# Performance work log

Hardware: AMD Instinct MI355X
Metric: run time of the kernel (lower is better)

Reference implementation:

```python
import jax, jax.numpy as jnp
import numpy as np

N = 4096
D = 256
THRESH = 0.04  # default threshold arg of MultiLayerGCN.forward


def setup_inputs() -> dict:
    key = jax.random.key(0)
    ks = jax.random.split(key, 6)
    A = jax.random.normal(ks[0], (N, N), dtype=jnp.float32)
    features = jax.random.normal(ks[1], (N, D), dtype=jnp.float32)
    s = 0.02
    W1 = jax.random.normal(ks[2], (D, D), dtype=jnp.float32) * s
    b1 = jax.random.normal(ks[3], (D,), dtype=jnp.float32) * s
    W2 = jax.random.normal(ks[4], (D, D), dtype=jnp.float32) * s
    b2 = jax.random.normal(ks[5], (D,), dtype=jnp.float32) * s
    return {"A": A, "features": features, "W1": W1, "b1": b1, "W2": W2, "b2": b2}


def _graph_conv(C, out_isqrt, in_isqrt, h, W, b):
    # DGL GraphConv, norm='both': scale src by out_deg^-1/2, aggregate over
    # edges u->v (rst[v] = sum_u C[u,v] * h[u]), scale dst by in_deg^-1/2.
    h = (h * out_isqrt[:, None]) @ W            # [N, out]
    agg = jnp.einsum('uv,ud->vd', C, h)          # C^T @ h, honoring edge direction
    return agg * in_isqrt[:, None] + b


def reference(A, features, W1, b1, W2, b2):
    dt = features.dtype
    mask = (A >= THRESH).astype(dt)
    # add_edges(nodes, nodes) adds self loops on top of surviving diagonal -> counts
    C = mask + jnp.eye(A.shape[0], dtype=dt)
    out_deg = jnp.maximum(C.sum(axis=1), 1.0)    # clamp(min=1) as in DGL
    in_deg = jnp.maximum(C.sum(axis=0), 1.0)
    out_isqrt = jax.lax.rsqrt(out_deg)
    in_isqrt = jax.lax.rsqrt(in_deg)
    h1 = jax.nn.relu(_graph_conv(C, out_isqrt, in_isqrt, features, W1, b1))
    h2 = jax.nn.relu(_graph_conv(C, out_isqrt, in_isqrt, h1, W2, b2))
    return (h1, h2)
```

## Files before the change

### kernel.cpp

```cpp
#include <hip/hip_runtime.h>
#include <stdint.h>

#define NN 4096
#define DD 256
#define TH 0.04f

typedef __attribute__((ext_vector_type(4))) float f32x4;
typedef __attribute__((ext_vector_type(16))) float f32x16;
typedef __attribute__((ext_vector_type(8))) short s16x8;
typedef unsigned short us;

__device__ __forceinline__ us f2bf(float f) {
  union { float f; uint32_t u; } x; x.f = f;
  uint32_t u = x.u;
  return (us)((u + 0x7FFFu + ((u >> 16) & 1u)) >> 16);
}
__device__ __forceinline__ float bf2f(us h) {
  union { uint32_t u; float f; } x; x.u = ((uint32_t)h) << 16;
  return x.f;
}

__device__ __forceinline__ void hw_block(const float* __restrict__ H,
                                         const float* __restrict__ W,
                                         int u0,
                                         us* __restrict__ hWb,
                                         us* __restrict__ hWbP,
                                         char* smem) {
  us (*hs)[264] = reinterpret_cast<us(*)[264]>(smem);
  us (*wt)[34]  = reinterpret_cast<us(*)[34]>(smem + 16 * 264 * 2);
  us (*lt)[260] = reinterpret_cast<us(*)[260]>(smem + 16 * 264 * 2 + 256 * 34 * 2);
  const int t = threadIdx.x;
#pragma unroll
  for (int rep = 0; rep < 4; ++rep) {
    const int flat = rep * 256 + t;
    const int row = flat >> 6, c4 = (flat & 63) * 4;
    f32x4 v = *reinterpret_cast<const f32x4*>(H + (size_t)(u0 + row) * DD + c4);
    uint2 pw;
    pw.x = (uint32_t)f2bf(v[0]) | ((uint32_t)f2bf(v[1]) << 16);
    pw.y = (uint32_t)f2bf(v[2]) | ((uint32_t)f2bf(v[3]) << 16);
    *reinterpret_cast<uint2*>(&hs[row][c4]) = pw;
  }
  const int lane = t & 63, w = t >> 6, l15 = lane & 15, l4 = lane >> 4;
  const f32x4 z = {0.f, 0.f, 0.f, 0.f};
  f32x4 acc[4];
#pragma unroll
  for (int jn = 0; jn < 4; ++jn) acc[jn] = z;
#pragma unroll 1
  for (int ks = 0; ks < 8; ++ks) {
    __syncthreads();
#pragma unroll
    for (int rr = 0; rr < 8; ++rr) {
      const int flat = rr * 256 + t;
      const int k = flat >> 6, d0 = (flat & 63) * 4;
      f32x4 wv = *reinterpret_cast<const f32x4*>(W + (size_t)(ks * 32 + k) * DD + d0);
      wt[d0 + 0][k] = f2bf(wv[0]);
      wt[d0 + 1][k] = f2bf(wv[1]);
      wt[d0 + 2][k] = f2bf(wv[2]);
      wt[d0 + 3][k] = f2bf(wv[3]);
    }
    __syncthreads();
    s16x8 af = *reinterpret_cast<const s16x8*>(&hs[l15][ks * 32 + l4 * 8]);
#pragma unroll
    for (int jn = 0; jn < 4; ++jn) {
      const int dt = w * 4 + jn;
      s16x8 bf = *reinterpret_cast<const s16x8*>(&wt[dt * 16 + l15][l4 * 8]);
      acc[jn] = __builtin_amdgcn_mfma_f32_16x16x32_bf16(af, bf, acc[jn], 0, 0, 0);
    }
  }
#pragma unroll
  for (int jn = 0; jn < 4; ++jn) {
    const int d = w * 64 + jn * 16 + l15;
#pragma unroll
    for (int r = 0; r < 4; ++r) {
      const int ul = l4 * 4 + r;
      us hv = f2bf(acc[jn][r]);
      hWb[(size_t)(u0 + ul) * DD + d] = hv;
      lt[ul][d] = hv;
    }
  }
  __syncthreads();
  const int sg = u0 >> 4;
#pragma unroll
  for (int cc = 0; cc < 2; ++cc) {
    const int c = t * 2 + cc;
    const int dt = c >> 6, lc = c & 63;
    const int ub = (lc >> 5) * 8;
    const int d = dt * 32 + (lc & 31);
    uint4 val;
    val.x = (uint32_t)lt[ub + 0][d] | ((uint32_t)lt[ub + 1][d] << 16);
    val.y = (uint32_t)lt[ub + 2][d] | ((uint32_t)lt[ub + 3][d] << 16);
    val.z = (uint32_t)lt[ub + 4][d] | ((uint32_t)lt[ub + 5][d] << 16);
    val.w = (uint32_t)lt[ub + 6][d] | ((uint32_t)lt[ub + 7][d] << 16);
    *reinterpret_cast<uint4*>(hWbP + ((size_t)dt * 256 + sg) * 512 + lc * 8) = val;
  }
}

__global__ __launch_bounds__(256) void k_scanhw1(const float* __restrict__ A,
                                                 const float* __restrict__ feat,
                                                 const float* __restrict__ W1,
                                                 us* __restrict__ bitsT,
                                                 unsigned char* __restrict__ colpart,
                                                 float* __restrict__ oif,
                                                 us* __restrict__ oib,
                                                 us* __restrict__ hWb,
                                                 us* __restrict__ hWbP) {
  __shared__ __align__(16) char smem[34176];
  if (blockIdx.x >= 512) {
    hw_block(feat, W1, (blockIdx.x - 512) * 16, hWb, hWbP, smem);
    return;
  }
  us* lds16 = reinterpret_cast<us*>(smem);
  const int t = threadIdx.x, b = blockIdx.x;
  const int u0 = b * 8;
  uint32_t cs[16];
#pragma unroll
  for (int k = 0; k < 16; ++k) cs[k] = 0;
#pragma unroll
  for (int rb = 0; rb < 2; ++rb) {
    f32x4 a[4][4];
#pragma unroll
    for (int r = 0; r < 4; ++r) {
      const f32x4* p = reinterpret_cast<const f32x4*>(A + (size_t)(u0 + rb * 4 + r) * NN + t * 16);
#pragma unroll
      for (int c = 0; c < 4; ++c) a[r][c] = p[c];
    }
#pragma unroll
    for (int r = 0; r < 4; ++r) {
      uint32_t m = 0;
#pragma unroll
      for (int c = 0; c < 4; ++c)
#pragma unroll
        for (int j = 0; j < 4; ++j) m |= (a[r][c][j] >= TH ? 1u : 0u) << (c * 4 + j);
      lds16[t * 8 + rb * 4 + r] = (us)m;
#pragma unroll
      for (int k = 0; k < 16; ++k) cs[k] += (m >> k) & 1u;
    }
  }
  uint4 pk;
  pk.x = cs[0]  | (cs[1]  << 8) | (cs[2]  << 16) | (cs[3]  << 24);
  pk.y = cs[4]  | (cs[5]  << 8) | (cs[6]  << 16) | (cs[7]  << 24);
  pk.z = cs[8]  | (cs[9]  << 8) | (cs[10] << 16) | (cs[11] << 24);
  pk.w = cs[12] | (cs[13] << 8) | (cs[14] << 16) | (cs[15] << 24);
  *reinterpret_cast<uint4*>(colpart + (size_t)b * 4096 + t * 16) = pk;
  __syncthreads();
  uint4 wv4 = *reinterpret_cast<const uint4*>(&lds16[t * 8]);
  *reinterpret_cast<uint4*>(bitsT + (size_t)t * 4096 + u0) = wv4;
  if (t < 64) {
    const int r = t >> 3, part = t & 7;
    uint32_t s = 0;
#pragma unroll
    for (int wv = part * 32; wv < part * 32 + 32; ++wv)
      s += (uint32_t)__popc((uint32_t)lds16[wv * 8 + r]);
    s += __shfl_down(s, 4, 8);
    s += __shfl_down(s, 2, 8);
    s += __shfl_down(s, 1, 8);
    if (part == 0) {
      float val = rsqrtf((float)(s + 1u));
      oif[u0 + r] = val;
      oib[u0 + r] = f2bf(val);
    }
  }
}

__global__ __launch_bounds__(256) void k_hw(const float* __restrict__ H,
                                            const float* __restrict__ W,
                                            us* __restrict__ hWb,
                                            us* __restrict__ hWbP) {
  __shared__ __align__(16) char smem[34176];
  hw_block(H, W, blockIdx.x * 16, hWb, hWbP, smem);
}

__global__ __launch_bounds__(512, 2) void k_spmm(const us* __restrict__ bitsT,
                                                 const us* __restrict__ hWbP,
                                                 const us* __restrict__ hWb,
                                                 const float* __restrict__ oif,
                                                 const us* __restrict__ oib,
                                                 const unsigned char* __restrict__ colpart,
                                                 float* __restrict__ ii_g,
                                                 const float* __restrict__ bias,
                                                 float* __restrict__ dst,
                                                 int doii) {
  __shared__ float lds[4 * 64 * 68];
  __shared__ float ii_s[64];
  const int t = threadIdx.x, bb = blockIdx.x;
  const int lane = t & 63, w = t >> 6;
  const int kc = w >> 1, dn = w & 1;
  const int xcd = bb & 7, jj = bb >> 3;
  const int vt = xcd * 8 + (jj >> 2), dq = jj & 3;
  const int V0 = vt * 64, D0 = dq * 64;

  if (doii) {
    uint32_t* sc = reinterpret_cast<uint32_t*>(lds);
    const int v4 = t & 15, c = t >> 4;
    uint32_t s0 = 0, s1 = 0;
#pragma unroll 4
    for (int r = 0; r < 16; ++r) {
      uint32_t x = *reinterpret_cast<const uint32_t*>(colpart + (size_t)(c * 16 + r) * 4096 + V0 + v4 * 4);
      s0 += x & 0x00FF00FFu;
      s1 += (x >> 8) & 0x00FF00FFu;
    }
    sc[(c * 16 + v4) * 2] = s0;
    sc[(c * 16 + v4) * 2 + 1] = s1;
    __syncthreads();
    if (t < 64) {
      const int v4b = t >> 2, sub = t & 3;
      const int reg = sub & 1, hi = sub >> 1;
      uint32_t s = 0;
#pragma unroll
      for (int cc = 0; cc < 32; ++cc)
        s += (sc[(cc * 16 + v4b) * 2 + reg] >> (hi * 16)) & 0xFFFFu;
      float val = rsqrtf((float)(s + 1u));
      ii_s[t] = val;
      ii_g[V0 + t] = val;
    }
    __syncthreads();
  } else {
    if (t < 64) ii_s[t] = ii_g[V0 + t];
    __syncthreads();
  }

  const int l31 = lane & 31, l5 = lane >> 5;
  const uint32_t sh = lane & 15;
  const int wsel = (lane >> 4) & 1;
  const us* A0 = bitsT + (size_t)(vt * 4 + wsel) * 4096 + kc * 1024 + l5 * 8;
  const us* A1 = bitsT + (size_t)(vt * 4 + 2 + wsel) * 4096 + kc * 1024 + l5 * 8;
  const us* Ob = oib + kc * 1024 + l5 * 8;
  const int dt = dq * 2 + dn;
  const us* Bp = hWbP + ((size_t)dt * 256 + kc * 64) * 512 + lane * 8;

  f32x16 acc0, acc1;
#pragma unroll
  for (int q = 0; q < 16; ++q) { acc0[q] = 0.f; acc1[q] = 0.f; }

  uint4 h0a = *reinterpret_cast<const uint4*>(A0);
  uint4 h1a = *reinterpret_cast<const uint4*>(A1);
  s16x8 oa = *reinterpret_cast<const s16x8*>(Ob);
  s16x8 pa = *reinterpret_cast<const s16x8*>(Bp);
  uint4 h0b = *reinterpret_cast<const uint4*>(A0 + 16);
  uint4 h1b = *reinterpret_cast<const uint4*>(A1 + 16);
  s16x8 ob = *reinterpret_cast<const s16x8*>(Ob + 16);
  s16x8 pb = *reinterpret_cast<const s16x8*>(Bp + 512);

#define XPAND(AF, H, O)                                                        \
  {                                                                            \
    const uint32_t* ou = reinterpret_cast<const uint32_t*>(&(O));              \
    uint32_t m_;                                                               \
    m_ = (((H).x >> sh) & 0x10001u) * 0xFFFFu; AF.u[0] = ou[0] & m_;           \
    m_ = (((H).y >> sh) & 0x10001u) * 0xFFFFu; AF.u[1] = ou[1] & m_;           \
    m_ = (((H).z >> sh) & 0x10001u) * 0xFFFFu; AF.u[2] = ou[2] & m_;           \
    m_ = (((H).w >> sh) & 0x10001u) * 0xFFFFu; AF.u[3] = ou[3] & m_;           \
  }

#pragma unroll 1
  for (int it = 0; it < 32; ++it) {
    {
      union { s16x8 v; uint32_t u[4]; } af0, af1;
      XPAND(af0, h0a, oa);
      XPAND(af1, h1a, oa);
      acc0 = __builtin_amdgcn_mfma_f32_32x32x16_bf16(af0.v, pa, acc0, 0, 0, 0);
      acc1 = __builtin_amdgcn_mfma_f32_32x32x16_bf16(af1.v, pa, acc1, 0, 0, 0);
      const int sA = (it * 2 + 2) & 63;
      h0a = *reinterpret_cast<const uint4*>(A0 + sA * 16);
      h1a = *reinterpret_cast<const uint4*>(A1 + sA * 16);
      oa = *reinterpret_cast<const s16x8*>(Ob + sA * 16);
      pa = *reinterpret_cast<const s16x8*>(Bp + (size_t)sA * 512);
    }
    {
      union { s16x8 v; uint32_t u[4]; } af0, af1;
      XPAND(af0, h0b, ob);
      XPAND(af1, h1b, ob);
      acc0 = __builtin_amdgcn_mfma_f32_32x32x16_bf16(af0.v, pb, acc0, 0, 0, 0);
      acc1 = __builtin_amdgcn_mfma_f32_32x32x16_bf16(af1.v, pb, acc1, 0, 0, 0);
      const int sB = (it * 2 + 3) & 63;
      h0b = *reinterpret_cast<const uint4*>(A0 + sB * 16);
      h1b = *reinterpret_cast<const uint4*>(A1 + sB * 16);
      ob = *reinterpret_cast<const s16x8*>(Ob + sB * 16);
      pb = *reinterpret_cast<const s16x8*>(Bp + (size_t)sB * 512);
    }
  }
#undef XPAND

  float* buf = lds + (size_t)kc * (64 * 68);
#pragma unroll
  for (int reg = 0; reg < 16; ++reg) {
    const int row = (reg & 3) + 8 * (reg >> 2) + 4 * l5;
    buf[row * 68 + dn * 32 + l31] = acc0[reg];
    buf[(32 + row) * 68 + dn * 32 + l31] = acc1[reg];
  }
  __syncthreads();

  const int vloc = t >> 3, d8 = (t & 7) * 8;
  const int v = V0 + vloc;
  const float* base = lds + vloc * 68 + d8;
  f32x4 s0v = *reinterpret_cast<const f32x4*>(base);
  f32x4 s1v = *reinterpret_cast<const f32x4*>(base + 4);
#pragma unroll
  for (int q = 1; q < 4; ++q) {
    s0v += *reinterpret_cast<const f32x4*>(base + q * (64 * 68));
    s1v += *reinterpret_cast<const f32x4*>(base + q * (64 * 68) + 4);
  }
  union { s16x8 v; us u[8]; } self;
  self.v = *reinterpret_cast<const s16x8*>(hWb + (size_t)v * DD + D0 + d8);
  const float iv = ii_s[vloc];
  const float ov = oif[v];
  const f32x4 bi0 = *reinterpret_cast<const f32x4*>(bias + D0 + d8);
  const f32x4 bi1 = *reinterpret_cast<const f32x4*>(bias + D0 + d8 + 4);
  f32x4 o0, o1;
#pragma unroll
  for (int e = 0; e < 4; ++e) {
    o0[e] = fmaxf((s0v[e] + ov * bf2f(self.u[e])) * iv + bi0[e], 0.f);
    o1[e] = fmaxf((s1v[e] + ov * bf2f(self.u[e + 4])) * iv + bi1[e], 0.f);
  }
  f32x4* po = reinterpret_cast<f32x4*>(dst + (size_t)v * DD + D0 + d8);
  po[0] = o0; po[1] = o1;
}

extern "C" void kernel_launch(void* const* d_in, const int* in_sizes, int n_in,
                              void* d_out, int out_size, void* d_ws, size_t ws_size,
                              hipStream_t stream) {
  const float* A    = (const float*)d_in[0];
  const float* feat = (const float*)d_in[1];
  const float* W1   = (const float*)d_in[2];
  const float* b1   = (const float*)d_in[3];
  const float* W2   = (const float*)d_in[4];
  const float* b2   = (const float*)d_in[5];
  float* out = (float*)d_out;
  char* ws = (char*)d_ws;

  us*            bitsT   = (us*)ws;
  unsigned char* colpart = (unsigned char*)(ws + (2u << 20));
  us*            hWbP    = (us*)(ws + (4u << 20));
  us*            hWb     = (us*)(ws + (6u << 20));
  float*         oif     = (float*)(ws + (8u << 20));
  us*            oib     = (us*)(ws + (8u << 20) + (16u << 10));
  float*         ii_g    = (float*)(ws + (8u << 20) + (24u << 10));

  k_scanhw1<<<768, 256, 0, stream>>>(A, feat, W1, bitsT, colpart, oif, oib, hWb, hWbP);
  k_spmm<<<256, 512, 0, stream>>>(bitsT, hWbP, hWb, oif, oib, colpart, ii_g, b1, out, 1);
  k_hw<<<256, 256, 0, stream>>>(out, W2, hWb, hWbP);
  k_spmm<<<256, 512, 0, stream>>>(bitsT, hWbP, hWb, oif, oib, colpart, ii_g, b2,
                                  out + (size_t)NN * DD, 0);
}
```

Before: 86.33 us.

## Pre-pack W2 into MFMA fragments and share A-fragment across two D tiles in SpMM

The first kernel now also converts W2 to bf16 in MFMA B-fragment order, and the layer-2 h·W kernel reads these fragments straight from global memory instead of staging and transposing W through LDS. The SpMM kernel is re-tiled so each wave builds one expanded adjacency fragment and reuses it for two D sub-tiles. This halves the bit-expansion ALU work and uses a 4-deep prefetch ring. The trade-off is more registers for the deeper prefetch and more global B-fragment loads per wave.

```diff
diff --git a/kernel.cpp b/kernel.cpp
--- a/kernel.cpp
+++ b/kernel.cpp
@@ -20,12 +20,12 @@
   return x.f;
 }
 
-__device__ __forceinline__ void hw_block(const float* __restrict__ H,
-                                         const float* __restrict__ W,
-                                         int u0,
-                                         us* __restrict__ hWb,
-                                         us* __restrict__ hWbP,
-                                         char* smem) {
+__device__ __forceinline__ void hw_selfstage(const float* __restrict__ H,
+                                             const float* __restrict__ W,
+                                             int u0,
+                                             us* __restrict__ hWb,
+                                             us* __restrict__ hWbP,
+                                             char* smem) {
   us (*hs)[264] = reinterpret_cast<us(*)[264]>(smem);
   us (*wt)[34]  = reinterpret_cast<us(*)[34]>(smem + 16 * 264 * 2);
   us (*lt)[260] = reinterpret_cast<us(*)[260]>(smem + 16 * 264 * 2 + 256 * 34 * 2);
@@ -98,15 +98,17 @@
 __global__ __launch_bounds__(256) void k_scanhw1(const float* __restrict__ A,
                                                  const float* __restrict__ feat,
                                                  const float* __restrict__ W1,
+                                                 const float* __restrict__ W2,
                                                  us* __restrict__ bitsT,
                                                  unsigned char* __restrict__ colpart,
                                                  float* __restrict__ oif,
                                                  us* __restrict__ oib,
                                                  us* __restrict__ hWb,
-                                                 us* __restrict__ hWbP) {
+                                                 us* __restrict__ hWbP,
+                                                 us* __restrict__ W2TbP) {
   __shared__ __align__(16) char smem[34176];
   if (blockIdx.x >= 512) {
-    hw_block(feat, W1, (blockIdx.x - 512) * 16, hWb, hWbP, smem);
+    hw_selfstage(feat, W1, (blockIdx.x - 512) * 16, hWb, hWbP, smem);
     return;
   }
   us* lds16 = reinterpret_cast<us*>(smem);
@@ -160,14 +162,81 @@
       oib[u0 + r] = f2bf(val);
     }
   }
-}
-
-__global__ __launch_bounds__(256) void k_hw(const float* __restrict__ H,
-                                            const float* __restrict__ W,
-                                            us* __restrict__ hWb,
-                                            us* __restrict__ hWbP) {
-  __shared__ __align__(16) char smem[34176];
-  hw_block(H, W, blockIdx.x * 16, hWb, hWbP, smem);
+  if (b < 16) {
+    const int base = b * 4096 + t * 16;
+#pragma unroll
+    for (int e = 0; e < 16; ++e) {
+      const int idx = base + e;
+      const int frag = idx >> 9, pos = idx & 511;
+      const int lc = pos >> 3, j = pos & 7;
+      const int dt = frag >> 3, ks = frag & 7;
+      const int k = ks * 32 + (lc >> 4) * 8 + j;
+      const int d = dt * 16 + (lc & 15);
+      W2TbP[idx] = f2bf(W2[k * 256 + d]);
+    }
+  }
+}
+
+__global__ __launch_bounds__(256) void k_hw2(const float* __restrict__ H,
+                                             const us* __restrict__ WP,
+                                             us* __restrict__ hWb,
+                                             us* __restrict__ hWbP) {
+  __shared__ us hs[16][264];
+  __shared__ us lt[16][260];
+  const int t = threadIdx.x;
+  const int u0 = blockIdx.x * 16;
+#pragma unroll
+  for (int rep = 0; rep < 4; ++rep) {
+    const int flat = rep * 256 + t;
+    const int row = flat >> 6, c4 = (flat & 63) * 4;
+    f32x4 v = *reinterpret_cast<const f32x4*>(H + (size_t)(u0 + row) * DD + c4);
+    uint2 pw;
+    pw.x = (uint32_t)f2bf(v[0]) | ((uint32_t)f2bf(v[1]) << 16);
+    pw.y = (uint32_t)f2bf(v[2]) | ((uint32_t)f2bf(v[3]) << 16);
+    *reinterpret_cast<uint2*>(&hs[row][c4]) = pw;
+  }
+  __syncthreads();
+  const int lane = t & 63, w = t >> 6, l15 = lane & 15, l4 = lane >> 4;
+  const f32x4 z = {0.f, 0.f, 0.f, 0.f};
+  f32x4 acc[4];
+#pragma unroll
+  for (int jn = 0; jn < 4; ++jn) acc[jn] = z;
+#pragma unroll
+  for (int ks = 0; ks < 8; ++ks) {
+    s16x8 af = *reinterpret_cast<const s16x8*>(&hs[l15][ks * 32 + l4 * 8]);
+#pragma unroll
+    for (int jn = 0; jn < 4; ++jn) {
+      const int dt = w * 4 + jn;
+      s16x8 bf = *reinterpret_cast<const s16x8*>(WP + ((size_t)dt * 8 + ks) * 512 + lane * 8);
+      acc[jn] = __builtin_amdgcn_mfma_f32_16x16x32_bf16(af, bf, acc[jn], 0, 0, 0);
+    }
+  }
+#pragma unroll
+  for (int jn = 0; jn < 4; ++jn) {
+    const int d = w * 64 + jn * 16 + l15;
+#pragma unroll
+    for (int r = 0; r < 4; ++r) {
+      const int ul = l4 * 4 + r;
+      us hv = f2bf(acc[jn][r]);
+      hWb[(size_t)(u0 + ul) * DD + d] = hv;
+      lt[ul][d] = hv;
+    }
+  }
+  __syncthreads();
+  const int sg = u0 >> 4;
+#pragma unroll
+  for (int cc = 0; cc < 2; ++cc) {
+    const int c = t * 2 + cc;
+    const int dt = c >> 6, lc = c & 63;
+    const int ub = (lc >> 5) * 8;
+    const int d = dt * 32 + (lc & 31);
+    uint4 val;
+    val.x = (uint32_t)lt[ub + 0][d] | ((uint32_t)lt[ub + 1][d] << 16);
+    val.y = (uint32_t)lt[ub + 2][d] | ((uint32_t)lt[ub + 3][d] << 16);
+    val.z = (uint32_t)lt[ub + 4][d] | ((uint32_t)lt[ub + 5][d] << 16);
+    val.w = (uint32_t)lt[ub + 6][d] | ((uint32_t)lt[ub + 7][d] << 16);
+    *reinterpret_cast<uint4*>(hWbP + ((size_t)dt * 256 + sg) * 512 + lc * 8) = val;
+  }
 }
 
 __global__ __launch_bounds__(512, 2) void k_spmm(const us* __restrict__ bitsT,
@@ -184,7 +253,7 @@
   __shared__ float ii_s[64];
   const int t = threadIdx.x, bb = blockIdx.x;
   const int lane = t & 63, w = t >> 6;
-  const int kc = w >> 1, dn = w & 1;
+  const int mi = w & 1, kc = w >> 1;
   const int xcd = bb & 7, jj = bb >> 3;
   const int vt = xcd * 8 + (jj >> 2), dq = jj & 3;
   const int V0 = vt * 64, D0 = dq * 64;
@@ -221,71 +290,52 @@
 
   const int l31 = lane & 31, l5 = lane >> 5;
   const uint32_t sh = lane & 15;
-  const int wsel = (lane >> 4) & 1;
-  const us* A0 = bitsT + (size_t)(vt * 4 + wsel) * 4096 + kc * 1024 + l5 * 8;
-  const us* A1 = bitsT + (size_t)(vt * 4 + 2 + wsel) * 4096 + kc * 1024 + l5 * 8;
+  const int wvl = vt * 4 + mi * 2 + ((lane >> 4) & 1);
+  const us* Ab = bitsT + (size_t)wvl * 4096 + kc * 1024 + l5 * 8;
   const us* Ob = oib + kc * 1024 + l5 * 8;
-  const int dt = dq * 2 + dn;
-  const us* Bp = hWbP + ((size_t)dt * 256 + kc * 64) * 512 + lane * 8;
+  const us* Bp0 = hWbP + ((size_t)(dq * 2 + 0) * 256 + kc * 64) * 512 + lane * 8;
+  const us* Bp1 = hWbP + ((size_t)(dq * 2 + 1) * 256 + kc * 64) * 512 + lane * 8;
 
   f32x16 acc0, acc1;
 #pragma unroll
   for (int q = 0; q < 16; ++q) { acc0[q] = 0.f; acc1[q] = 0.f; }
 
-  uint4 h0a = *reinterpret_cast<const uint4*>(A0);
-  uint4 h1a = *reinterpret_cast<const uint4*>(A1);
-  s16x8 oa = *reinterpret_cast<const s16x8*>(Ob);
-  s16x8 pa = *reinterpret_cast<const s16x8*>(Bp);
-  uint4 h0b = *reinterpret_cast<const uint4*>(A0 + 16);
-  uint4 h1b = *reinterpret_cast<const uint4*>(A1 + 16);
-  s16x8 ob = *reinterpret_cast<const s16x8*>(Ob + 16);
-  s16x8 pb = *reinterpret_cast<const s16x8*>(Bp + 512);
-
-#define XPAND(AF, H, O)                                                        \
-  {                                                                            \
-    const uint32_t* ou = reinterpret_cast<const uint32_t*>(&(O));              \
-    uint32_t m_;                                                               \
-    m_ = (((H).x >> sh) & 0x10001u) * 0xFFFFu; AF.u[0] = ou[0] & m_;           \
-    m_ = (((H).y >> sh) & 0x10001u) * 0xFFFFu; AF.u[1] = ou[1] & m_;           \
-    m_ = (((H).z >> sh) & 0x10001u) * 0xFFFFu; AF.u[2] = ou[2] & m_;           \
-    m_ = (((H).w >> sh) & 0x10001u) * 0xFFFFu; AF.u[3] = ou[3] & m_;           \
+  uint4 h[4]; s16x8 o[4], p0[4], p1[4];
+#pragma unroll
+  for (int sl = 0; sl < 4; ++sl) {
+    h[sl]  = *reinterpret_cast<const uint4*>(Ab + sl * 16);
+    o[sl]  = *reinterpret_cast<const s16x8*>(Ob + sl * 16);
+    p0[sl] = *reinterpret_cast<const s16x8*>(Bp0 + (size_t)sl * 512);
+    p1[sl] = *reinterpret_cast<const s16x8*>(Bp1 + (size_t)sl * 512);
   }
 
 #pragma unroll 1
-  for (int it = 0; it < 32; ++it) {
-    {
-      union { s16x8 v; uint32_t u[4]; } af0, af1;
-      XPAND(af0, h0a, oa);
-      XPAND(af1, h1a, oa);
-      acc0 = __builtin_amdgcn_mfma_f32_32x32x16_bf16(af0.v, pa, acc0, 0, 0, 0);
-      acc1 = __builtin_amdgcn_mfma_f32_32x32x16_bf16(af1.v, pa, acc1, 0, 0, 0);
-      const int sA = (it * 2 + 2) & 63;
-      h0a = *reinterpret_cast<const uint4*>(A0 + sA * 16);
-      h1a = *reinterpret_cast<const uint4*>(A1 + sA * 16);
-      oa = *reinterpret_cast<const s16x8*>(Ob + sA * 16);
-      pa = *reinterpret_cast<const s16x8*>(Bp + (size_t)sA * 512);
-    }
-    {
-      union { s16x8 v; uint32_t u[4]; } af0, af1;
-      XPAND(af0, h0b, ob);
-      XPAND(af1, h1b, ob);
-      acc0 = __builtin_amdgcn_mfma_f32_32x32x16_bf16(af0.v, pb, acc0, 0, 0, 0);
-      acc1 = __builtin_amdgcn_mfma_f32_32x32x16_bf16(af1.v, pb, acc1, 0, 0, 0);
-      const int sB = (it * 2 + 3) & 63;
-      h0b = *reinterpret_cast<const uint4*>(A0 + sB * 16);
-      h1b = *reinterpret_cast<const uint4*>(A1 + sB * 16);
-      ob = *reinterpret_cast<const s16x8*>(Ob + sB * 16);
-      pb = *reinterpret_cast<const s16x8*>(Bp + (size_t)sB * 512);
-    }
-  }
-#undef XPAND
+  for (int it = 0; it < 16; ++it) {
+#pragma unroll
+    for (int sl = 0; sl < 4; ++sl) {
+      union { s16x8 v; uint32_t u[4]; } af;
+      const uint32_t* ou = reinterpret_cast<const uint32_t*>(&o[sl]);
+      uint32_t m;
+      m = ((h[sl].x >> sh) & 0x10001u) * 0xFFFFu; af.u[0] = ou[0] & m;
+      m = ((h[sl].y >> sh) & 0x10001u) * 0xFFFFu; af.u[1] = ou[1] & m;
+      m = ((h[sl].z >> sh) & 0x10001u) * 0xFFFFu; af.u[2] = ou[2] & m;
+      m = ((h[sl].w >> sh) & 0x10001u) * 0xFFFFu; af.u[3] = ou[3] & m;
+      acc0 = __builtin_amdgcn_mfma_f32_32x32x16_bf16(af.v, p0[sl], acc0, 0, 0, 0);
+      acc1 = __builtin_amdgcn_mfma_f32_32x32x16_bf16(af.v, p1[sl], acc1, 0, 0, 0);
+      const int ns = (it * 4 + sl + 4) & 63;
+      h[sl]  = *reinterpret_cast<const uint4*>(Ab + ns * 16);
+      o[sl]  = *reinterpret_cast<const s16x8*>(Ob + ns * 16);
+      p0[sl] = *reinterpret_cast<const s16x8*>(Bp0 + (size_t)ns * 512);
+      p1[sl] = *reinterpret_cast<const s16x8*>(Bp1 + (size_t)ns * 512);
+    }
+  }
 
   float* buf = lds + (size_t)kc * (64 * 68);
 #pragma unroll
   for (int reg = 0; reg < 16; ++reg) {
     const int row = (reg & 3) + 8 * (reg >> 2) + 4 * l5;
-    buf[row * 68 + dn * 32 + l31] = acc0[reg];
-    buf[(32 + row) * 68 + dn * 32 + l31] = acc1[reg];
+    buf[(mi * 32 + row) * 68 + l31] = acc0[reg];
+    buf[(mi * 32 + row) * 68 + 32 + l31] = acc1[reg];
   }
   __syncthreads();
 
@@ -331,13 +381,15 @@
   unsigned char* colpart = (unsigned char*)(ws + (2u << 20));
   us*            hWbP    = (us*)(ws + (4u << 20));
   us*            hWb     = (us*)(ws + (6u << 20));
-  float*         oif     = (float*)(ws + (8u << 20));
-  us*            oib     = (us*)(ws + (8u << 20) + (16u << 10));
-  float*         ii_g    = (float*)(ws + (8u << 20) + (24u << 10));
-
-  k_scanhw1<<<768, 256, 0, stream>>>(A, feat, W1, bitsT, colpart, oif, oib, hWb, hWbP);
+  us*            W2TbP   = (us*)(ws + (8u << 20));
+  float*         oif     = (float*)(ws + (8u << 20) + (1u << 17));
+  us*            oib     = (us*)(ws + (8u << 20) + (1u << 17) + (16u << 10));
+  float*         ii_g    = (float*)(ws + (8u << 20) + (1u << 17) + (24u << 10));
+
+  k_scanhw1<<<768, 256, 0, stream>>>(A, feat, W1, W2, bitsT, colpart, oif, oib,
+                                     hWb, hWbP, W2TbP);
   k_spmm<<<256, 512, 0, stream>>>(bitsT, hWbP, hWb, oif, oib, colpart, ii_g, b1, out, 1);
-  k_hw<<<256, 256, 0, stream>>>(out, W2, hWb, hWbP);
+  k_hw2<<<256, 256, 0, stream>>>(out, W2TbP, hWb, hWbP);
   k_spmm<<<256, 512, 0, stream>>>(bitsT, hWbP, hWb, oif, oib, colpart, ii_g, b2,
                                   out + (size_t)NN * DD, 0);
 }
```

Measured after the change: 79.97 us. 1.08x faster.
